# Optimization experiments

Measured on AMD Instinct MI355X. Metric: run time of the kernel, lower is better.

The kernel has to match this reference:

```python
import jax, jax.numpy as jnp
import numpy as np

C = 256; HEADS = 8; LEVELS = 4; POINTS = 4; D = C // HEADS
SPATIAL = np.array([[96, 96], [48, 48], [24, 24], [12, 12]], dtype=np.int32)  # (H, W) per level
AREAS = SPATIAL[:, 0] * SPATIAL[:, 1]
HW = int(AREAS.sum())  # 12240
LSI = np.concatenate([[0], np.cumsum(AREAS)[:-1]]).astype(np.int32)
N = 1; Q = HW


def setup_inputs() -> dict:
    key = jax.random.key(0)
    ks = jax.random.split(key, 12)
    s = 0.02
    return {
        "query": jax.random.normal(ks[0], (N, Q, C), jnp.float32),
        "reference_points": jax.random.uniform(ks[1], (N, Q, LEVELS, 2), jnp.float32),
        "input_flatten": jax.random.normal(ks[2], (N, HW, C), jnp.float32),
        "input_spatial_shapes": jnp.asarray(SPATIAL),
        "input_level_start_index": jnp.asarray(LSI),
        "W_off": jax.random.normal(ks[3], (C, HEADS * LEVELS * POINTS * 2), jnp.float32) * s,
        "b_off": jax.random.normal(ks[4], (HEADS * LEVELS * POINTS * 2,), jnp.float32) * s,
        "W_attn": jax.random.normal(ks[5], (C, HEADS * LEVELS * POINTS), jnp.float32) * s,
        "b_attn": jax.random.normal(ks[6], (HEADS * LEVELS * POINTS,), jnp.float32) * s,
        "W_val": jax.random.normal(ks[7], (C, C), jnp.float32) * (1.0 / np.sqrt(C)),
        "b_val": jax.random.normal(ks[8], (C,), jnp.float32) * s,
        "W_out": jax.random.normal(ks[9], (C, C), jnp.float32) * (1.0 / np.sqrt(C)),
        "b_out": jax.random.normal(ks[10], (C,), jnp.float32) * s,
    }


def _ms_deform_attn(query, reference_points, input_flatten, sp, lsi,
                    W_off, b_off, W_attn, b_attn, W_val, b_val, W_out, b_out):
    n, q, c = query.shape
    hw = input_flatten.shape[1]
    # value projection -> [N, Hd, HW, D]
    value = (input_flatten @ W_val + b_val).reshape(n, hw, HEADS, D).transpose(0, 2, 1, 3)
    # sampling offsets [N,Q,Hd,L,P,2]
    off = (query @ W_off + b_off).reshape(n, q, HEADS, LEVELS, POINTS, 2)
    # attention weights softmaxed over L*P (done inside the fused CUDA kernel)
    attn = jax.nn.softmax((query @ W_attn + b_attn).reshape(n, q, HEADS, LEVELS * POINTS), axis=-1)
    attn = attn.reshape(n, q, HEADS, LEVELS, POINTS)
    # normalized sampling locations (reference_points last dim == 2 branch)
    norm = jnp.stack([sp[:, 1], sp[:, 0]], -1).astype(query.dtype)  # (W, H) per level
    loc = reference_points[:, :, None, :, None, :] + off / norm[None, None, None, :, None, :]
    Hl = sp[:, 0][None, None, None, :, None]
    Wl = sp[:, 1][None, None, None, :, None]
    start = lsi[None, None, None, :, None]
    # grid_sample-style (align_corners=False) pixel coordinates
    x = loc[..., 0] * Wl - 0.5
    y = loc[..., 1] * Hl - 0.5
    x0 = jnp.floor(x); y0 = jnp.floor(y)
    lx = x - x0; ly = y - y0
    x0i = x0.astype(jnp.int32); y0i = y0.astype(jnp.int32)

    def gather(yi, xi):
        valid = (xi >= 0) & (xi < Wl) & (yi >= 0) & (yi < Hl)
        idx = jnp.where(valid, start + yi * Wl + xi, 0)  # [N,Q,Hd,L,P]
        idx_t = idx.transpose(0, 2, 1, 3, 4).reshape(n, HEADS, q * LEVELS * POINTS, 1)
        g = jnp.take_along_axis(value, idx_t, axis=2)  # [N,Hd,Q*L*P,D]
        g = g.reshape(n, HEADS, q, LEVELS, POINTS, D)
        return g * valid.transpose(0, 2, 1, 3, 4)[..., None]

    def w(a):
        return a.transpose(0, 2, 1, 3, 4)[..., None]  # [N,Hd,Q,L,P,1]

    sampled = (gather(y0i, x0i) * w((1 - ly) * (1 - lx))
               + gather(y0i, x0i + 1) * w((1 - ly) * lx)
               + gather(y0i + 1, x0i) * w(ly * (1 - lx))
               + gather(y0i + 1, x0i + 1) * w(ly * lx))  # [N,Hd,Q,L,P,D]
    out = jnp.einsum('nhqlpd,nqhlp->nqhd', sampled, attn).reshape(n, q, c)
    return out @ W_out + b_out


def reference(query, reference_points, input_flatten, input_spatial_shapes, input_level_start_index,
              W_off, b_off, W_attn, b_attn, W_val, b_val, W_out, b_out):
    return _ms_deform_attn(query, reference_points, input_flatten,
                           input_spatial_shapes, input_level_start_index,
                           W_off, b_off, W_attn, b_attn, W_val, b_val, W_out, b_out)
```

## Files before the change

kernel.cpp:

```cpp
#include <hip/hip_runtime.h>

#define QTOT 12240
#define KD   256

typedef float f32x4 __attribute__((ext_vector_type(4)));
typedef short s16x8 __attribute__((ext_vector_type(8)));
typedef short s16x4 __attribute__((ext_vector_type(4)));
typedef unsigned short ushort_t;

__device__ __forceinline__ unsigned short f2b(float x) {
    union { float f; unsigned u; } c; c.f = x;
    unsigned r = c.u + 0x7fffu + ((c.u >> 16) & 1u);
    return (unsigned short)(r >> 16);
}
__device__ __forceinline__ int swz(int row, int kb) { return row * 512 + (kb ^ ((row & 7) << 4)); }

__global__ __launch_bounds__(256) void prep(
    const float* __restrict__ W_val, const float* __restrict__ W_off,
    const float* __restrict__ W_attn, const float* __restrict__ W_out,
    const float* __restrict__ b_off, const float* __restrict__ b_attn,
    ushort_t* __restrict__ WvT, ushort_t* __restrict__ WcT,
    ushort_t* __restrict__ WoT, float* __restrict__ bcomb)
{
    int id = blockIdx.x * 256 + threadIdx.x;
    if (id < 65536) { int n = id >> 8, k = id & 255; WvT[id] = f2b(W_val[k * 256 + n]); }
    else if (id < 163840) {
        int t = id - 65536; int n = t >> 8, k = t & 255;
        float v = (n < 256) ? W_off[k * 256 + n] : W_attn[k * 128 + (n - 256)];
        WcT[t] = f2b(v);
    } else if (id < 229376) {
        int t = id - 163840; int n = t >> 8, k = t & 255;
        WoT[t] = f2b(W_out[k * 256 + n]);
    } else if (id < 229760) {
        int t = id - 229376; bcomb[t] = (t < 256) ? b_off[t] : b_attn[t - 256];
    }
}

__global__ __launch_bounds__(256) void gemm1(
    const float* __restrict__ inflat, const float* __restrict__ query,
    const ushort_t* __restrict__ WvT, const ushort_t* __restrict__ WcT,
    const float* __restrict__ b_val, const float* __restrict__ bcomb,
    ushort_t* __restrict__ projb, ushort_t* __restrict__ offb,
    float* __restrict__ logitf)
{
    __shared__ char As[16384];
    const int b = blockIdx.x;
    const bool isval = b < 383;
    const int bm = (isval ? b : b - 383) * 32;
    const float* A = isval ? inflat : query;
    const ushort_t* WT = isval ? WvT : WcT;
    const int nc = isval ? 4 : 6;

    const int tid = threadIdx.x, lane = tid & 63, wave = tid >> 6;
    const int lr = lane & 15, g8 = (lane >> 4) * 8;

    {
        const float4* srcb = (const float4*)(A + (size_t)bm * KD);
        const int rem_rows = QTOT - bm;
#pragma unroll
        for (int j = 0; j < 8; ++j) {
            const int f4i = j * 256 + tid;
            const int row = f4i >> 6;
            const int colb = (f4i & 63) * 8;
            float4 f = make_float4(0.f, 0.f, 0.f, 0.f);
            if (row < rem_rows) f = srcb[f4i];
            s16x4 v;
            v[0] = f2b(f.x); v[1] = f2b(f.y); v[2] = f2b(f.z); v[3] = f2b(f.w);
            *(s16x4*)(As + swz(row, colb)) = v;
        }
    }
    __syncthreads();

    const int rg = (lane >> 4) * 4;

    for (int c = 0; c < nc; ++c) {
        const int col = c * 64 + wave * 16 + lr;
        s16x8 bfr[8];
        {
            const ushort_t* bp = WT + (size_t)col * KD + g8;
#pragma unroll
            for (int kc = 0; kc < 8; ++kc) bfr[kc] = *(const s16x8*)(bp + kc * 32);
        }
        f32x4 acc[2];
        acc[0] = (f32x4)0.f; acc[1] = (f32x4)0.f;
#pragma unroll
        for (int kc = 0; kc < 8; ++kc) {
            const int kb = (kc * 32 + g8) * 2;
            s16x8 a0 = *(const s16x8*)(As + swz(lr,      kb));
            s16x8 a1 = *(const s16x8*)(As + swz(16 + lr, kb));
            acc[0] = __builtin_amdgcn_mfma_f32_16x16x32_bf16(a0, bfr[kc], acc[0], 0, 0, 0);
            acc[1] = __builtin_amdgcn_mfma_f32_16x16x32_bf16(a1, bfr[kc], acc[1], 0, 0, 0);
        }
        const float bb = isval ? b_val[col] : bcomb[col];
#pragma unroll
        for (int mf = 0; mf < 2; ++mf)
#pragma unroll
            for (int rr = 0; rr < 4; ++rr) {
                const int row = bm + mf * 16 + rg + rr;
                if (row >= QTOT) continue;
                const float v = acc[mf][rr] + bb;
                if (isval)          projb[(size_t)row * 256 + col] = f2b(v);
                else if (col < 256) offb [(size_t)row * 256 + col] = f2b(v);
                else                logitf[(size_t)row * 128 + col - 256] = v;
            }
    }
}

__global__ __launch_bounds__(256) void sample5(
    const float* __restrict__ rp, const ushort_t* __restrict__ offb,
    const float* __restrict__ logitf, const ushort_t* __restrict__ projb,
    const int* __restrict__ sp, const int* __restrict__ lsi,
    ushort_t* __restrict__ outpre)
{
    const int q0 = blockIdx.x * 4;
    const int tid = threadIdx.x;

    __shared__ int   s_idx[512][4];
    __shared__ float s_w[512][4];

#pragma unroll
    for (int rep = 0; rep < 2; ++rep) {
        const int task = rep * 256 + tid;
        const int ql = task >> 7, t = task & 127;
        const int l = (t >> 2) & 3;
        const int q = q0 + ql;

        float logit = logitf[(size_t)q * 128 + t];
        float mx = logit;
#pragma unroll
        for (int d = 1; d < 16; d <<= 1) mx = fmaxf(mx, __shfl_xor(mx, d));
        float e = __expf(logit - mx);
        float s = e;
#pragma unroll
        for (int d = 1; d < 16; d <<= 1) s += __shfl_xor(s, d);
        const float aw = e / s;

        const unsigned opk = *(const unsigned*)&offb[(size_t)q * 256 + t * 2];
        const float ox = __uint_as_float(opk << 16);
        const float oy = __uint_as_float(opk & 0xffff0000u);

        const int Hl = sp[l * 2], Wl = sp[l * 2 + 1], st = lsi[l];
        const float rx = rp[((size_t)q * 4 + l) * 2 + 0];
        const float ry = rp[((size_t)q * 4 + l) * 2 + 1];

        const float x = rx * (float)Wl + ox - 0.5f;
        const float y = ry * (float)Hl + oy - 0.5f;
        const float xf = floorf(x), yf = floorf(y);
        const int x0 = (int)xf, y0 = (int)yf;
        const float lx = x - xf, ly = y - yf;

        const bool vx0 = (x0 >= 0) && (x0 < Wl);
        const bool vx1 = (x0 + 1 >= 0) && (x0 + 1 < Wl);
        const bool vy0 = (y0 >= 0) && (y0 < Hl);
        const bool vy1 = (y0 + 1 >= 0) && (y0 + 1 < Hl);

        s_w[task][0] = (vx0 && vy0) ? aw * (1.f - ly) * (1.f - lx) : 0.f;
        s_w[task][1] = (vx1 && vy0) ? aw * (1.f - ly) * lx         : 0.f;
        s_w[task][2] = (vx0 && vy1) ? aw * ly * (1.f - lx)         : 0.f;
        s_w[task][3] = (vx1 && vy1) ? aw * ly * lx                 : 0.f;
        s_idx[task][0] = (vx0 && vy0) ? (st + y0 * Wl + x0) * 512           : 0;
        s_idx[task][1] = (vx1 && vy0) ? (st + y0 * Wl + x0 + 1) * 512       : 0;
        s_idx[task][2] = (vx0 && vy1) ? (st + (y0 + 1) * Wl + x0) * 512     : 0;
        s_idx[task][3] = (vx1 && vy1) ? (st + (y0 + 1) * Wl + x0 + 1) * 512 : 0;
    }
    __syncthreads();

    const int t = tid & 127, qlA = tid >> 7;
    const int h = t >> 4, pq = (t >> 2) & 3, c8 = t & 3;
    const char* basec = (const char*)projb + (h * 32 + c8 * 8) * 2;

    float aA[8] = {0,0,0,0,0,0,0,0};
    float aB[8] = {0,0,0,0,0,0,0,0};
#pragma unroll
    for (int l = 0; l < 4; ++l) {
        const int slotA = (qlA << 7)       + h * 16 + l * 4 + pq;
        const int slotB = ((qlA + 2) << 7) + h * 16 + l * 4 + pq;
        const int4   iA = *(const int4*)s_idx[slotA];
        const float4 wA = *(const float4*)s_w[slotA];
        const int4   iB = *(const int4*)s_idx[slotB];
        const float4 wB = *(const float4*)s_w[slotB];
#pragma unroll
        for (int c = 0; c < 4; ++c) {
            const int   idA = (c == 0) ? iA.x : (c == 1) ? iA.y : (c == 2) ? iA.z : iA.w;
            const float wwA = (c == 0) ? wA.x : (c == 1) ? wA.y : (c == 2) ? wA.z : wA.w;
            const uint4 v = *(const uint4*)(basec + idA);
            aA[0] += wwA * __uint_as_float(v.x << 16);
            aA[1] += wwA * __uint_as_float(v.x & 0xffff0000u);
            aA[2] += wwA * __uint_as_float(v.y << 16);
            aA[3] += wwA * __uint_as_float(v.y & 0xffff0000u);
            aA[4] += wwA * __uint_as_float(v.z << 16);
            aA[5] += wwA * __uint_as_float(v.z & 0xffff0000u);
            aA[6] += wwA * __uint_as_float(v.w << 16);
            aA[7] += wwA * __uint_as_float(v.w & 0xffff0000u);
        }
#pragma unroll
        for (int c = 0; c < 4; ++c) {
            const int   idB = (c == 0) ? iB.x : (c == 1) ? iB.y : (c == 2) ? iB.z : iB.w;
            const float wwB = (c == 0) ? wB.x : (c == 1) ? wB.y : (c == 2) ? wB.z : wB.w;
            const uint4 v = *(const uint4*)(basec + idB);
            aB[0] += wwB * __uint_as_float(v.x << 16);
            aB[1] += wwB * __uint_as_float(v.x & 0xffff0000u);
            aB[2] += wwB * __uint_as_float(v.y << 16);
            aB[3] += wwB * __uint_as_float(v.y & 0xffff0000u);
            aB[4] += wwB * __uint_as_float(v.z << 16);
            aB[5] += wwB * __uint_as_float(v.z & 0xffff0000u);
            aB[6] += wwB * __uint_as_float(v.w << 16);
            aB[7] += wwB * __uint_as_float(v.w & 0xffff0000u);
        }
    }
#pragma unroll
    for (int i = 0; i < 8; ++i) {
        aA[i] += __shfl_xor(aA[i], 4);  aA[i] += __shfl_xor(aA[i], 8);
        aB[i] += __shfl_xor(aB[i], 4);  aB[i] += __shfl_xor(aB[i], 8);
    }
    if (pq == 0) {
        const int colo = h * 32 + c8 * 8;
        uint4 o;
        o.x = (unsigned)f2b(aA[0]) | ((unsigned)f2b(aA[1]) << 16);
        o.y = (unsigned)f2b(aA[2]) | ((unsigned)f2b(aA[3]) << 16);
        o.z = (unsigned)f2b(aA[4]) | ((unsigned)f2b(aA[5]) << 16);
        o.w = (unsigned)f2b(aA[6]) | ((unsigned)f2b(aA[7]) << 16);
        *(uint4*)&outpre[(size_t)(q0 + qlA) * 256 + colo] = o;
        o.x = (unsigned)f2b(aB[0]) | ((unsigned)f2b(aB[1]) << 16);
        o.y = (unsigned)f2b(aB[2]) | ((unsigned)f2b(aB[3]) << 16);
        o.z = (unsigned)f2b(aB[4]) | ((unsigned)f2b(aB[5]) << 16);
        o.w = (unsigned)f2b(aB[6]) | ((unsigned)f2b(aB[7]) << 16);
        *(uint4*)&outpre[(size_t)(q0 + qlA + 2) * 256 + colo] = o;
    }
}

__global__ __launch_bounds__(256) void gemm_o(
    const ushort_t* __restrict__ Ab, const ushort_t* __restrict__ WoT,
    const float* __restrict__ b_out, float* __restrict__ out)
{
    const int bm = blockIdx.x * 32;
    const int tid = threadIdx.x, lane = tid & 63, wave = tid >> 6;
    const int lr = lane & 15, g8 = (lane >> 4) * 8;
    const int rg = (lane >> 4) * 4;

    const ushort_t* ap0;
    const ushort_t* ap1;
    {
        int r0 = bm + lr;      if (r0 >= QTOT) r0 = QTOT - 1;
        int r1 = bm + 16 + lr; if (r1 >= QTOT) r1 = QTOT - 1;
        ap0 = Ab + (size_t)r0 * KD + g8;
        ap1 = Ab + (size_t)r1 * KD + g8;
    }

#pragma unroll
    for (int c = 0; c < 4; ++c) {
        const int col = c * 64 + wave * 16 + lr;
        s16x8 bfr[8];
        {
            const ushort_t* bp = WoT + (size_t)col * KD + g8;
#pragma unroll
            for (int kc = 0; kc < 8; ++kc) bfr[kc] = *(const s16x8*)(bp + kc * 32);
        }
        f32x4 acc[2];
        acc[0] = (f32x4)0.f; acc[1] = (f32x4)0.f;
#pragma unroll
        for (int kc = 0; kc < 8; ++kc) {
            s16x8 a0 = *(const s16x8*)(ap0 + kc * 32);
            s16x8 a1 = *(const s16x8*)(ap1 + kc * 32);
            acc[0] = __builtin_amdgcn_mfma_f32_16x16x32_bf16(a0, bfr[kc], acc[0], 0, 0, 0);
            acc[1] = __builtin_amdgcn_mfma_f32_16x16x32_bf16(a1, bfr[kc], acc[1], 0, 0, 0);
        }
        const float bb = b_out[col];
#pragma unroll
        for (int mf = 0; mf < 2; ++mf)
#pragma unroll
            for (int rr = 0; rr < 4; ++rr) {
                const int row = bm + mf * 16 + rg + rr;
                if (row < QTOT) out[(size_t)row * 256 + col] = acc[mf][rr] + bb;
            }
    }
}

extern "C" void kernel_launch(void* const* d_in, const int* in_sizes, int n_in,
                              void* d_out, int out_size, void* d_ws, size_t ws_size,
                              hipStream_t stream) {
    const float* query  = (const float*)d_in[0];
    const float* rp     = (const float*)d_in[1];
    const float* inflat = (const float*)d_in[2];
    const int*   sp     = (const int*)d_in[3];
    const int*   lsi    = (const int*)d_in[4];
    const float* W_off  = (const float*)d_in[5];
    const float* b_off  = (const float*)d_in[6];
    const float* W_attn = (const float*)d_in[7];
    const float* b_attn = (const float*)d_in[8];
    const float* W_val  = (const float*)d_in[9];
    const float* b_val  = (const float*)d_in[10];
    const float* W_out  = (const float*)d_in[11];
    const float* b_out  = (const float*)d_in[12];
    float* out = (float*)d_out;

    char* ws = (char*)d_ws;
    ushort_t* projb  = (ushort_t*)ws; ws += (size_t)QTOT * 256 * 2;
    ushort_t* offb   = (ushort_t*)ws; ws += (size_t)QTOT * 256 * 2;
    float*    logitf = (float*)ws;    ws += (size_t)QTOT * 128 * 4;
    ushort_t* outpre = (ushort_t*)ws; ws += (size_t)QTOT * 256 * 2;
    ushort_t* WvT    = (ushort_t*)ws; ws += 65536 * 2;
    ushort_t* WcT    = (ushort_t*)ws; ws += 98304 * 2;
    ushort_t* WoT    = (ushort_t*)ws; ws += 65536 * 2;
    float*    bcomb  = (float*)ws;    ws += 384 * 4;

    prep<<<dim3(898), dim3(256), 0, stream>>>(W_val, W_off, W_attn, W_out, b_off, b_attn,
                                              WvT, WcT, WoT, bcomb);

    gemm1<<<dim3(766), dim3(256), 0, stream>>>(inflat, query, WvT, WcT, b_val, bcomb,
                                               projb, offb, logitf);

    sample5<<<dim3(3060), dim3(256), 0, stream>>>(rp, offb, logitf, projb, sp, lsi, outpre);

    gemm_o<<<dim3(383), dim3(256), 0, stream>>>(outpre, WoT, b_out, out);
}
```

Measured before the change: 69.72 us.

## Split sampling blocks by head half, eight queries per block

Each sampling block now covers 8 queries for one half of the heads (4 heads), where it used to cover 4 queries for all 8 heads. The first 1530 blocks take heads 0-3 and the rest take heads 4-7. Each thread now accumulates one query with two points per level, not two queries with one point each, and the cross-lane reduction drops from two shuffle steps to one. The aim is to improve gather locality for each head-half's value channels and to cut register and shuffle cost, at the price of reading reference points and level data twice per query.

```diff
diff --git a/kernel.cpp b/kernel.cpp
--- a/kernel.cpp
+++ b/kernel.cpp
@@ -106,13 +106,16 @@
     }
 }
 
-__global__ __launch_bounds__(256) void sample5(
+__global__ __launch_bounds__(256) void sample6(
     const float* __restrict__ rp, const ushort_t* __restrict__ offb,
     const float* __restrict__ logitf, const ushort_t* __restrict__ projb,
     const int* __restrict__ sp, const int* __restrict__ lsi,
     ushort_t* __restrict__ outpre)
 {
-    const int q0 = blockIdx.x * 4;
+    const int bid = blockIdx.x;
+    const int hh = (bid >= 1530) ? 1 : 0;
+    const int g  = hh ? (bid - 1530) : bid;
+    const int q0 = g * 8;
     const int tid = threadIdx.x;
 
     __shared__ int   s_idx[512][4];
@@ -121,11 +124,15 @@
 #pragma unroll
     for (int rep = 0; rep < 2; ++rep) {
         const int task = rep * 256 + tid;
-        const int ql = task >> 7, t = task & 127;
-        const int l = (t >> 2) & 3;
+        const int ql = task >> 6;
+        const int hp = (task >> 4) & 3;
+        const int lp = task & 15;
+        const int l = lp >> 2;
         const int q = q0 + ql;
-
-        float logit = logitf[(size_t)q * 128 + t];
+        const int gh = hh * 4 + hp;
+        const int t128 = gh * 16 + lp;
+
+        float logit = logitf[(size_t)q * 128 + t128];
         float mx = logit;
 #pragma unroll
         for (int d = 1; d < 16; d <<= 1) mx = fmaxf(mx, __shfl_xor(mx, d));
@@ -135,7 +142,7 @@
         for (int d = 1; d < 16; d <<= 1) s += __shfl_xor(s, d);
         const float aw = e / s;
 
-        const unsigned opk = *(const unsigned*)&offb[(size_t)q * 256 + t * 2];
+        const unsigned opk = *(const unsigned*)&offb[(size_t)q * 256 + t128 * 2];
         const float ox = __uint_as_float(opk << 16);
         const float oy = __uint_as_float(opk & 0xffff0000u);
 
@@ -165,67 +172,50 @@
     }
     __syncthreads();
 
-    const int t = tid & 127, qlA = tid >> 7;
-    const int h = t >> 4, pq = (t >> 2) & 3, c8 = t & 3;
-    const char* basec = (const char*)projb + (h * 32 + c8 * 8) * 2;
-
-    float aA[8] = {0,0,0,0,0,0,0,0};
-    float aB[8] = {0,0,0,0,0,0,0,0};
+    const int c8 = tid & 3;
+    const int pq = (tid >> 2) & 1;
+    const int hp = (tid >> 3) & 3;
+    const int ql = tid >> 5;
+    const int gh = hh * 4 + hp;
+    const char* basec = (const char*)projb + (gh * 32 + c8 * 8) * 2;
+    const int slot0 = (ql << 6) | (hp << 4);
+
+    float a0 = 0, a1 = 0, a2 = 0, a3 = 0, a4 = 0, a5 = 0, a6 = 0, a7 = 0;
 #pragma unroll
     for (int l = 0; l < 4; ++l) {
-        const int slotA = (qlA << 7)       + h * 16 + l * 4 + pq;
-        const int slotB = ((qlA + 2) << 7) + h * 16 + l * 4 + pq;
-        const int4   iA = *(const int4*)s_idx[slotA];
-        const float4 wA = *(const float4*)s_w[slotA];
-        const int4   iB = *(const int4*)s_idx[slotB];
-        const float4 wB = *(const float4*)s_w[slotB];
-#pragma unroll
-        for (int c = 0; c < 4; ++c) {
-            const int   idA = (c == 0) ? iA.x : (c == 1) ? iA.y : (c == 2) ? iA.z : iA.w;
-            const float wwA = (c == 0) ? wA.x : (c == 1) ? wA.y : (c == 2) ? wA.z : wA.w;
-            const uint4 v = *(const uint4*)(basec + idA);
-            aA[0] += wwA * __uint_as_float(v.x << 16);
-            aA[1] += wwA * __uint_as_float(v.x & 0xffff0000u);
-            aA[2] += wwA * __uint_as_float(v.y << 16);
-            aA[3] += wwA * __uint_as_float(v.y & 0xffff0000u);
-            aA[4] += wwA * __uint_as_float(v.z << 16);
-            aA[5] += wwA * __uint_as_float(v.z & 0xffff0000u);
-            aA[6] += wwA * __uint_as_float(v.w << 16);
-            aA[7] += wwA * __uint_as_float(v.w & 0xffff0000u);
-        }
-#pragma unroll
-        for (int c = 0; c < 4; ++c) {
-            const int   idB = (c == 0) ? iB.x : (c == 1) ? iB.y : (c == 2) ? iB.z : iB.w;
-            const float wwB = (c == 0) ? wB.x : (c == 1) ? wB.y : (c == 2) ? wB.z : wB.w;
-            const uint4 v = *(const uint4*)(basec + idB);
-            aB[0] += wwB * __uint_as_float(v.x << 16);
-            aB[1] += wwB * __uint_as_float(v.x & 0xffff0000u);
-            aB[2] += wwB * __uint_as_float(v.y << 16);
-            aB[3] += wwB * __uint_as_float(v.y & 0xffff0000u);
-            aB[4] += wwB * __uint_as_float(v.z << 16);
-            aB[5] += wwB * __uint_as_float(v.z & 0xffff0000u);
-            aB[6] += wwB * __uint_as_float(v.w << 16);
-            aB[7] += wwB * __uint_as_float(v.w & 0xffff0000u);
-        }
-    }
-#pragma unroll
-    for (int i = 0; i < 8; ++i) {
-        aA[i] += __shfl_xor(aA[i], 4);  aA[i] += __shfl_xor(aA[i], 8);
-        aB[i] += __shfl_xor(aB[i], 4);  aB[i] += __shfl_xor(aB[i], 8);
-    }
+#pragma unroll
+        for (int j = 0; j < 2; ++j) {
+            const int slot = slot0 | (l << 2) | (pq * 2 + j);
+            const int4   i4 = *(const int4*)s_idx[slot];
+            const float4 w4 = *(const float4*)s_w[slot];
+#pragma unroll
+            for (int c = 0; c < 4; ++c) {
+                const int   id = (c == 0) ? i4.x : (c == 1) ? i4.y : (c == 2) ? i4.z : i4.w;
+                const float w  = (c == 0) ? w4.x : (c == 1) ? w4.y : (c == 2) ? w4.z : w4.w;
+                const uint4 v = *(const uint4*)(basec + id);
+                a0 += w * __uint_as_float(v.x << 16);
+                a1 += w * __uint_as_float(v.x & 0xffff0000u);
+                a2 += w * __uint_as_float(v.y << 16);
+                a3 += w * __uint_as_float(v.y & 0xffff0000u);
+                a4 += w * __uint_as_float(v.z << 16);
+                a5 += w * __uint_as_float(v.z & 0xffff0000u);
+                a6 += w * __uint_as_float(v.w << 16);
+                a7 += w * __uint_as_float(v.w & 0xffff0000u);
+            }
+        }
+    }
+    a0 += __shfl_xor(a0, 4); a1 += __shfl_xor(a1, 4);
+    a2 += __shfl_xor(a2, 4); a3 += __shfl_xor(a3, 4);
+    a4 += __shfl_xor(a4, 4); a5 += __shfl_xor(a5, 4);
+    a6 += __shfl_xor(a6, 4); a7 += __shfl_xor(a7, 4);
+
     if (pq == 0) {
-        const int colo = h * 32 + c8 * 8;
         uint4 o;
-        o.x = (unsigned)f2b(aA[0]) | ((unsigned)f2b(aA[1]) << 16);
-        o.y = (unsigned)f2b(aA[2]) | ((unsigned)f2b(aA[3]) << 16);
-        o.z = (unsigned)f2b(aA[4]) | ((unsigned)f2b(aA[5]) << 16);
-        o.w = (unsigned)f2b(aA[6]) | ((unsigned)f2b(aA[7]) << 16);
-        *(uint4*)&outpre[(size_t)(q0 + qlA) * 256 + colo] = o;
-        o.x = (unsigned)f2b(aB[0]) | ((unsigned)f2b(aB[1]) << 16);
-        o.y = (unsigned)f2b(aB[2]) | ((unsigned)f2b(aB[3]) << 16);
-        o.z = (unsigned)f2b(aB[4]) | ((unsigned)f2b(aB[5]) << 16);
-        o.w = (unsigned)f2b(aB[6]) | ((unsigned)f2b(aB[7]) << 16);
-        *(uint4*)&outpre[(size_t)(q0 + qlA + 2) * 256 + colo] = o;
+        o.x = (unsigned)f2b(a0) | ((unsigned)f2b(a1) << 16);
+        o.y = (unsigned)f2b(a2) | ((unsigned)f2b(a3) << 16);
+        o.z = (unsigned)f2b(a4) | ((unsigned)f2b(a5) << 16);
+        o.w = (unsigned)f2b(a6) | ((unsigned)f2b(a7) << 16);
+        *(uint4*)&outpre[(size_t)(q0 + ql) * 256 + gh * 32 + c8 * 8] = o;
     }
 }
 
@@ -310,7 +300,7 @@
     gemm1<<<dim3(766), dim3(256), 0, stream>>>(inflat, query, WvT, WcT, b_val, bcomb,
                                                projb, offb, logitf);
 
-    sample5<<<dim3(3060), dim3(256), 0, stream>>>(rp, offb, logitf, projb, sp, lsi, outpre);
+    sample6<<<dim3(3060), dim3(256), 0, stream>>>(rp, offb, logitf, projb, sp, lsi, outpre);
 
     gemm_o<<<dim3(383), dim3(256), 0, stream>>>(outpre, WoT, b_out, out);
 }
```

Measured after the change: 68.93 us. No clear change (-1.1%).
